# Performance work log

Measured on AMD Instinct MI355X. Metric: run time of the kernel, lower is better.

## Reference

```python
import jax, jax.numpy as jnp
import numpy as np

NEG_BIG = -9e15  # matches torch's -9000000000000000.0 mask value
LEAKY_SLOPE = 0.2  # alpha passed to nn.LeakyReLU


def setup_inputs() -> dict:
    key = jax.random.key(0)
    k1, k2, k3, k4, k5 = jax.random.split(key, 5)
    N, din, de, dout = 500, 100, 200, 100
    return {
        "input_relations": jax.random.normal(k1, (N, din), dtype=jnp.float32),
        "input_entity_embeds": jax.random.normal(k2, (N, N, de), dtype=jnp.float32),
        "relation_adj": jax.random.randint(k3, (N, N), 0, 2, dtype=jnp.int32),
        "a": jax.random.normal(k4, (dout, 2 * din + de), dtype=jnp.float32) * 0.05,
        "a_2": jax.random.normal(k5, (1, dout), dtype=jnp.float32) * 0.05,
    }


def reference(input_relations, input_entity_embeds, relation_adj, a, a_2):
    # Faithful to: a_input[k=(i,j)] = concat(rel_i, rel_j, ent[i,j]); e = a @ a_input
    # We avoid materializing the (N*N, 2*din+de) concat by splitting `a` into the
    # three blocks that hit rel_i, rel_j and ent[i,j] respectively.
    N, din = input_relations.shape
    de = input_entity_embeds.shape[-1]
    a_src = a[:, :din]          # (dout, din) acts on rel_i
    a_dst = a[:, din:2 * din]   # (dout, din) acts on rel_j
    a_ent = a[:, 2 * din:]      # (dout, de)  acts on ent[i,j]

    # e[i, j, o] = a @ concat(rel_i, rel_j, ent_ij)   -> (N, N, dout)
    e = (
        (input_relations @ a_src.T)[:, None, :]
        + (input_relations @ a_dst.T)[None, :, :]
        + jnp.einsum("ijd,od->ijo", input_entity_embeds.reshape(N, N, de), a_ent)
    )

    # scalar score per pair, leaky relu, masked softmax over neighbors j (dim=1)
    e2 = jax.nn.leaky_relu(e @ a_2[0], LEAKY_SLOPE)  # (N, N)
    scores = jnp.where(relation_adj > 0, e2, jnp.float32(NEG_BIG))
    attention = jax.nn.softmax(scores, axis=1)  # (N, N)

    # weighted sum of the score features e (note: original multiplies attention by e,
    # the pre-leakyrelu linear scores, not by a transformed h)
    h_prime = jnp.einsum("ij,ijo->io", attention, e)  # (N, dout)
    return jax.nn.elu(h_prime)  # concat=True branch
```

## Files before the change

### kernel.cpp

```cpp
#include <hip/hip_runtime.h>
#include <stdint.h>
#include <math.h>

#define N     500
#define DIN   100
#define DE    200
#define DOUT  100
#define AROW  (2*DIN + DE)
#define SLOPE 0.2f

#define JCH   4
#define CROWS 125
#define KP    512
#define BK    720
#define DEP   208
#define GZF   104000

typedef __attribute__((ext_vector_type(8)))  short short8;
typedef __attribute__((ext_vector_type(16))) float f32x16;

static __device__ __forceinline__ unsigned short f2bf(float f) {
  union { float f; uint32_t u; } v; v.f = f;
  uint32_t r = (v.u + 0x7FFFu + ((v.u >> 16) & 1u)) >> 16;
  return (unsigned short)r;
}

__global__ __launch_bounds__(256)
void setup_kernel(const float* __restrict__ R, const float* __restrict__ A,
                  const float* __restrict__ a2,
                  float* __restrict__ src, float* __restrict__ ssrc,
                  float* __restrict__ sdst, float* __restrict__ wv,
                  unsigned short* __restrict__ Bcat, unsigned short* __restrict__ Pbuf,
                  float* __restrict__ gsum, float* __restrict__ Zsum) {
  int b = blockIdx.x, t = threadIdx.x;
  if (b < N) {
    int i = b;
    __shared__ float rrow[DIN];
    __shared__ float sred[4];
    if (t < DIN) rrow[t] = R[i * DIN + t];
    if (t < KP - N) Pbuf[i * KP + N + t] = 0;
    __syncthreads();
    int o = -1; bool isSrc = false;
    if (t < DOUT) { o = t; isSrc = true; }
    else if (t >= 128 && t < 128 + DOUT) { o = t - 128; }
    float val = 0.f;
    if (o >= 0) {
      const float* arow = A + o * AROW + (isSrc ? 0 : DIN);
      #pragma unroll 4
      for (int d = 0; d < DIN; ++d) val += rrow[d] * arow[d];
      if (isSrc) src[i * DOUT + o] = val;
      else       Bcat[o * BK + i] = f2bf(val);
    }
    float red = (o >= 0) ? val * a2[o] : 0.f;
    #pragma unroll
    for (int k = 1; k < 64; k <<= 1) red += __shfl_xor(red, k, 64);
    if ((t & 63) == 0) sred[t >> 6] = red;
    __syncthreads();
    if (t == 0)   ssrc[i] = sred[0] + sred[1];
    if (t == 128) sdst[i] = sred[2] + sred[3];
  } else if (b == N) {
    if (t < DE) {
      float s = 0.f;
      for (int o = 0; o < DOUT; ++o) s += A[o * AROW + 2 * DIN + t] * a2[o];
      wv[t] = s;
    }
  } else if (b <= N + DOUT) {
    int o = b - (N + 1);
    if (t < DE) Bcat[o * BK + KP + t] = f2bf(A[o * AROW + 2 * DIN + t]);
    if (t < KP - N) Bcat[o * BK + N + t] = 0;
    if (t >= 32 && t < 32 + (BK - KP - DE)) Bcat[o * BK + KP + DE + (t - 32)] = 0;
  } else if (b <= 702) {
    int off = (b - 601) * 1024 + t * 4;
    if (off < GZF) *(float4*)(gsum + off) = make_float4(0.f, 0.f, 0.f, 0.f);
  } else {
    if (t < 125) *(float4*)(Zsum + t * 4) = make_float4(0.f, 0.f, 0.f, 0.f);
  }
}

__global__ __launch_bounds__(256)
void passA(const float* __restrict__ E, const int* __restrict__ adj,
           const float* __restrict__ ssrcA, const float* __restrict__ sdstA,
           const float* __restrict__ wv,
           unsigned short* __restrict__ Pbuf,
           float* __restrict__ gsum, float* __restrict__ Zsum) {
  __shared__ int list[128];
  __shared__ int cntS;
  __shared__ float gl[4][200];
  __shared__ float zl[4];

  int bid = blockIdx.x;
  int i = bid >> 2, c = bid & 3;
  int jbeg = c * CROWS;
  int t = threadIdx.x, wid = t >> 6, lane = t & 63;

  if (t == 0) cntS = 0;
  __syncthreads();

  bool active = false;
  if (t < CROWS) active = (adj[(size_t)i * N + jbeg + t] > 0);
  unsigned long long mask = __ballot(active);
  int wbase = 0;
  if (lane == 0 && mask) wbase = atomicAdd(&cntS, __popcll(mask));
  wbase = __shfl(wbase, 0);
  if (active) {
    list[wbase + __popcll(mask & ((1ull << lane) - 1ull))] = jbeg + t;
  } else if (t < CROWS) {
    Pbuf[i * KP + jbeg + t] = 0;
  }
  __syncthreads();
  int cnt = cntS;

  float4 w4 = make_float4(0.f, 0.f, 0.f, 0.f);
  if (lane < 50) w4 = *(const float4*)(wv + lane * 4);
  float4 g = make_float4(0.f, 0.f, 0.f, 0.f);
  float Z = 0.f;
  float ssrc_i = ssrcA[i];
  const float* Erow = E + (size_t)i * N * DE;

  for (int base = wid * 4; base + 3 < cnt; base += 16) {
    int j0 = list[base], j1 = list[base + 1], j2 = list[base + 2], j3 = list[base + 3];
    float4 e0 = make_float4(0.f,0.f,0.f,0.f), e1 = e0, e2v = e0, e3 = e0;
    if (lane < 50) {
      e0  = *(const float4*)(Erow + (size_t)j0 * DE + lane * 4);
      e1  = *(const float4*)(Erow + (size_t)j1 * DE + lane * 4);
      e2v = *(const float4*)(Erow + (size_t)j2 * DE + lane * 4);
      e3  = *(const float4*)(Erow + (size_t)j3 * DE + lane * 4);
    }
    float d0 = e0.x*w4.x + e0.y*w4.y + e0.z*w4.z + e0.w*w4.w;
    float d1 = e1.x*w4.x + e1.y*w4.y + e1.z*w4.z + e1.w*w4.w;
    float d2 = e2v.x*w4.x + e2v.y*w4.y + e2v.z*w4.z + e2v.w*w4.w;
    float d3 = e3.x*w4.x + e3.y*w4.y + e3.z*w4.z + e3.w*w4.w;
    #pragma unroll
    for (int k = 1; k < 64; k <<= 1) {
      d0 += __shfl_xor(d0, k); d1 += __shfl_xor(d1, k);
      d2 += __shfl_xor(d2, k); d3 += __shfl_xor(d3, k);
    }
    float s0 = ssrc_i + sdstA[j0] + d0; s0 = s0 > 0.f ? s0 : SLOPE * s0;
    float s1 = ssrc_i + sdstA[j1] + d1; s1 = s1 > 0.f ? s1 : SLOPE * s1;
    float s2 = ssrc_i + sdstA[j2] + d2; s2 = s2 > 0.f ? s2 : SLOPE * s2;
    float s3 = ssrc_i + sdstA[j3] + d3; s3 = s3 > 0.f ? s3 : SLOPE * s3;
    float p0 = __expf(s0), p1 = __expf(s1), p2 = __expf(s2), p3 = __expf(s3);
    Z += (p0 + p1) + (p2 + p3);
    g.x += p0*e0.x + p1*e1.x + p2*e2v.x + p3*e3.x;
    g.y += p0*e0.y + p1*e1.y + p2*e2v.y + p3*e3.y;
    g.z += p0*e0.z + p1*e1.z + p2*e2v.z + p3*e3.z;
    g.w += p0*e0.w + p1*e1.w + p2*e2v.w + p3*e3.w;
    if (lane == 0) {
      Pbuf[i * KP + j0] = f2bf(p0); Pbuf[i * KP + j1] = f2bf(p1);
      Pbuf[i * KP + j2] = f2bf(p2); Pbuf[i * KP + j3] = f2bf(p3);
    }
  }
  for (int idx = (cnt & ~3) + wid; idx < cnt; idx += 4) {
    int j = list[idx];
    float4 ev = make_float4(0.f,0.f,0.f,0.f);
    if (lane < 50) ev = *(const float4*)(Erow + (size_t)j * DE + lane * 4);
    float d = ev.x*w4.x + ev.y*w4.y + ev.z*w4.z + ev.w*w4.w;
    #pragma unroll
    for (int k = 1; k < 64; k <<= 1) d += __shfl_xor(d, k);
    float s = ssrc_i + sdstA[j] + d; s = s > 0.f ? s : SLOPE * s;
    float p = __expf(s);
    Z += p;
    g.x += p*ev.x; g.y += p*ev.y; g.z += p*ev.z; g.w += p*ev.w;
    if (lane == 0) Pbuf[i * KP + j] = f2bf(p);
  }

  if (lane < 50) *(float4*)&gl[wid][lane * 4] = g;
  if (lane == 0) zl[wid] = Z;
  __syncthreads();
  if (t < 200) {
    float s = gl[0][t] + gl[1][t] + gl[2][t] + gl[3][t];
    atomicAdd(gsum + (size_t)i * DEP + t, s);
  }
  if (t == 200) atomicAdd(Zsum + i, zl[0] + zl[1] + zl[2] + zl[3]);
}

__global__ __launch_bounds__(256)
void combine_kernel(const float* __restrict__ src,
                    const unsigned short* __restrict__ Pbuf,
                    const unsigned short* __restrict__ Bcat,
                    const float* __restrict__ gsum,
                    const float* __restrict__ Zsum,
                    float* __restrict__ out) {
  int b = blockIdx.x;
  int t = threadIdx.x;
  int i0 = b * 32;
  int wave = t >> 6, lane = t & 63, c31 = lane & 31, hi = lane >> 5;
  int o = wave * 32 + c31;
  int arow = i0 + c31; if (arow > N - 1) arow = N - 1;

  const unsigned short* Prow = Pbuf + (size_t)arow * KP;
  const float* grow = gsum + (size_t)arow * DEP;

  f32x16 acc = {};
  #pragma unroll
  for (int ks = 0; ks < 45; ++ks) {
    short8 a, bf;
    if (ks < 32) {
      a = *(const short8*)(Prow + ks * 16 + hi * 8);
    } else {
      int d0 = (ks - 32) * 16 + hi * 8;
      float4 ga = *(const float4*)(grow + d0);
      float4 gb = *(const float4*)(grow + d0 + 4);
      a[0] = (short)f2bf(ga.x); a[1] = (short)f2bf(ga.y);
      a[2] = (short)f2bf(ga.z); a[3] = (short)f2bf(ga.w);
      a[4] = (short)f2bf(gb.x); a[5] = (short)f2bf(gb.y);
      a[6] = (short)f2bf(gb.z); a[7] = (short)f2bf(gb.w);
    }
    if (o < DOUT) bf = *(const short8*)(Bcat + (size_t)o * BK + ks * 16 + hi * 8);
    else { short8 zz = {}; bf = zz; }
    acc = __builtin_amdgcn_mfma_f32_32x32x16_bf16(a, bf, acc, 0, 0, 0);
  }

  if (o < DOUT) {
    #pragma unroll
    for (int r = 0; r < 16; ++r) {
      int row = (r & 3) + 8 * (r >> 2) + 4 * hi;
      int i = i0 + row;
      if (i < N) {
        float h = src[i * DOUT + o] + acc[r] / Zsum[i];
        out[i * DOUT + o] = h > 0.f ? h : expm1f(h);
      }
    }
  }
}

extern "C" void kernel_launch(void* const* d_in, const int* in_sizes, int n_in,
                              void* d_out, int out_size, void* d_ws, size_t ws_size,
                              hipStream_t stream) {
  const float* R   = (const float*)d_in[0];
  const float* E   = (const float*)d_in[1];
  const int*   adj = (const int*)d_in[2];
  const float* A   = (const float*)d_in[3];
  const float* a2  = (const float*)d_in[4];
  float* out = (float*)d_out;

  char* wsb = (char*)d_ws;
  float*          src  = (float*)(wsb + 0);
  float*          ssrc = (float*)(wsb + 200000);
  float*          sdst = (float*)(wsb + 202000);
  float*          wv   = (float*)(wsb + 204000);
  unsigned short* Bcat = (unsigned short*)(wsb + 204800);
  unsigned short* Pbuf = (unsigned short*)(wsb + 348800);
  float*          gsum = (float*)(wsb + 860800);
  float*          Zsum = (float*)(wsb + 1276800);

  setup_kernel<<<704, 256, 0, stream>>>(R, A, a2, src, ssrc, sdst, wv, Bcat, Pbuf, gsum, Zsum);
  passA<<<N * JCH, 256, 0, stream>>>(E, adj, ssrc, sdst, wv, Pbuf, gsum, Zsum);
  combine_kernel<<<16, 256, 0, stream>>>(src, Pbuf, Bcat, gsum, Zsum, out);
}
```

Measured before the change: 57.53 us.

## Halve passA blocks per row, unroll 8 neighbors, precompute bias, split combine into waves

passA now splits each row into 2 chunks of 250 instead of 4 of 125. Each wave processes 8 neighbor rows per iteration, which puts more E loads in flight. The per-neighbor bias (ssrc_i + sdst_j) is precomputed into shared memory while the compaction list is built. combine_kernel is relaunched as 64 single-wave blocks instead of 16 four-wave blocks, spreading the MFMA work over more CUs. Risks are higher register pressure from the 8 float4 buffers and fewer blocks for latency hiding in passA.

```diff
diff --git a/kernel.cpp b/kernel.cpp
--- a/kernel.cpp
+++ b/kernel.cpp
@@ -9,8 +9,8 @@
 #define AROW  (2*DIN + DE)
 #define SLOPE 0.2f
 
-#define JCH   4
-#define CROWS 125
+#define JCH   2
+#define CROWS 250
 #define KP    512
 #define BK    720
 #define DEP   208
@@ -77,25 +77,27 @@
   }
 }
 
-__global__ __launch_bounds__(256)
+__global__ __launch_bounds__(256, 4)
 void passA(const float* __restrict__ E, const int* __restrict__ adj,
            const float* __restrict__ ssrcA, const float* __restrict__ sdstA,
            const float* __restrict__ wv,
            unsigned short* __restrict__ Pbuf,
            float* __restrict__ gsum, float* __restrict__ Zsum) {
-  __shared__ int list[128];
+  __shared__ int list[CROWS + 6];
+  __shared__ float bias[CROWS + 6];
   __shared__ int cntS;
   __shared__ float gl[4][200];
   __shared__ float zl[4];
 
   int bid = blockIdx.x;
-  int i = bid >> 2, c = bid & 3;
+  int i = bid >> 1, c = bid & 1;
   int jbeg = c * CROWS;
   int t = threadIdx.x, wid = t >> 6, lane = t & 63;
 
   if (t == 0) cntS = 0;
   __syncthreads();
 
+  float ssrc_i = ssrcA[i];
   bool active = false;
   if (t < CROWS) active = (adj[(size_t)i * N + jbeg + t] > 0);
   unsigned long long mask = __ballot(active);
@@ -103,7 +105,9 @@
   if (lane == 0 && mask) wbase = atomicAdd(&cntS, __popcll(mask));
   wbase = __shfl(wbase, 0);
   if (active) {
-    list[wbase + __popcll(mask & ((1ull << lane) - 1ull))] = jbeg + t;
+    int slot = wbase + __popcll(mask & ((1ull << lane) - 1ull));
+    list[slot] = jbeg + t;
+    bias[slot] = ssrc_i + sdstA[jbeg + t];
   } else if (t < CROWS) {
     Pbuf[i * KP + jbeg + t] = 0;
   }
@@ -114,53 +118,63 @@
   if (lane < 50) w4 = *(const float4*)(wv + lane * 4);
   float4 g = make_float4(0.f, 0.f, 0.f, 0.f);
   float Z = 0.f;
-  float ssrc_i = ssrcA[i];
   const float* Erow = E + (size_t)i * N * DE;
 
-  for (int base = wid * 4; base + 3 < cnt; base += 16) {
-    int j0 = list[base], j1 = list[base + 1], j2 = list[base + 2], j3 = list[base + 3];
-    float4 e0 = make_float4(0.f,0.f,0.f,0.f), e1 = e0, e2v = e0, e3 = e0;
+  for (int base = wid * 8; base + 7 < cnt; base += 32) {
+    int jr[8];
+    float bi[8];
+    #pragma unroll
+    for (int r = 0; r < 8; ++r) { jr[r] = list[base + r]; bi[r] = bias[base + r]; }
+    float4 ev[8];
     if (lane < 50) {
-      e0  = *(const float4*)(Erow + (size_t)j0 * DE + lane * 4);
-      e1  = *(const float4*)(Erow + (size_t)j1 * DE + lane * 4);
-      e2v = *(const float4*)(Erow + (size_t)j2 * DE + lane * 4);
-      e3  = *(const float4*)(Erow + (size_t)j3 * DE + lane * 4);
-    }
-    float d0 = e0.x*w4.x + e0.y*w4.y + e0.z*w4.z + e0.w*w4.w;
-    float d1 = e1.x*w4.x + e1.y*w4.y + e1.z*w4.z + e1.w*w4.w;
-    float d2 = e2v.x*w4.x + e2v.y*w4.y + e2v.z*w4.z + e2v.w*w4.w;
-    float d3 = e3.x*w4.x + e3.y*w4.y + e3.z*w4.z + e3.w*w4.w;
+      #pragma unroll
+      for (int r = 0; r < 8; ++r)
+        ev[r] = *(const float4*)(Erow + (size_t)jr[r] * DE + lane * 4);
+    } else {
+      #pragma unroll
+      for (int r = 0; r < 8; ++r) ev[r] = make_float4(0.f, 0.f, 0.f, 0.f);
+    }
+    float d[8];
+    #pragma unroll
+    for (int r = 0; r < 8; ++r)
+      d[r] = ev[r].x * w4.x + ev[r].y * w4.y + ev[r].z * w4.z + ev[r].w * w4.w;
     #pragma unroll
     for (int k = 1; k < 64; k <<= 1) {
-      d0 += __shfl_xor(d0, k); d1 += __shfl_xor(d1, k);
-      d2 += __shfl_xor(d2, k); d3 += __shfl_xor(d3, k);
-    }
-    float s0 = ssrc_i + sdstA[j0] + d0; s0 = s0 > 0.f ? s0 : SLOPE * s0;
-    float s1 = ssrc_i + sdstA[j1] + d1; s1 = s1 > 0.f ? s1 : SLOPE * s1;
-    float s2 = ssrc_i + sdstA[j2] + d2; s2 = s2 > 0.f ? s2 : SLOPE * s2;
-    float s3 = ssrc_i + sdstA[j3] + d3; s3 = s3 > 0.f ? s3 : SLOPE * s3;
-    float p0 = __expf(s0), p1 = __expf(s1), p2 = __expf(s2), p3 = __expf(s3);
-    Z += (p0 + p1) + (p2 + p3);
-    g.x += p0*e0.x + p1*e1.x + p2*e2v.x + p3*e3.x;
-    g.y += p0*e0.y + p1*e1.y + p2*e2v.y + p3*e3.y;
-    g.z += p0*e0.z + p1*e1.z + p2*e2v.z + p3*e3.z;
-    g.w += p0*e0.w + p1*e1.w + p2*e2v.w + p3*e3.w;
+      #pragma unroll
+      for (int r = 0; r < 8; ++r) d[r] += __shfl_xor(d[r], k);
+    }
+    float p[8];
+    float zacc = 0.f;
+    #pragma unroll
+    for (int r = 0; r < 8; ++r) {
+      float s = bi[r] + d[r];
+      s = s > 0.f ? s : SLOPE * s;
+      p[r] = __expf(s);
+      zacc += p[r];
+    }
+    Z += zacc;
+    #pragma unroll
+    for (int r = 0; r < 8; ++r) {
+      g.x += p[r] * ev[r].x; g.y += p[r] * ev[r].y;
+      g.z += p[r] * ev[r].z; g.w += p[r] * ev[r].w;
+    }
     if (lane == 0) {
-      Pbuf[i * KP + j0] = f2bf(p0); Pbuf[i * KP + j1] = f2bf(p1);
-      Pbuf[i * KP + j2] = f2bf(p2); Pbuf[i * KP + j3] = f2bf(p3);
-    }
-  }
-  for (int idx = (cnt & ~3) + wid; idx < cnt; idx += 4) {
+      #pragma unroll
+      for (int r = 0; r < 8; ++r) Pbuf[i * KP + jr[r]] = f2bf(p[r]);
+    }
+  }
+  for (int idx = (cnt & ~7) + wid; idx < cnt; idx += 4) {
     int j = list[idx];
-    float4 ev = make_float4(0.f,0.f,0.f,0.f);
+    float bi = bias[idx];
+    float4 ev = make_float4(0.f, 0.f, 0.f, 0.f);
     if (lane < 50) ev = *(const float4*)(Erow + (size_t)j * DE + lane * 4);
-    float d = ev.x*w4.x + ev.y*w4.y + ev.z*w4.z + ev.w*w4.w;
+    float d = ev.x * w4.x + ev.y * w4.y + ev.z * w4.z + ev.w * w4.w;
     #pragma unroll
     for (int k = 1; k < 64; k <<= 1) d += __shfl_xor(d, k);
-    float s = ssrc_i + sdstA[j] + d; s = s > 0.f ? s : SLOPE * s;
+    float s = bi + d; s = s > 0.f ? s : SLOPE * s;
     float p = __expf(s);
     Z += p;
-    g.x += p*ev.x; g.y += p*ev.y; g.z += p*ev.z; g.w += p*ev.w;
+    g.x += p * ev.x; g.y += p * ev.y; g.z += p * ev.z; g.w += p * ev.w;
     if (lane == 0) Pbuf[i * KP + j] = f2bf(p);
   }
 
@@ -174,7 +188,7 @@
   if (t == 200) atomicAdd(Zsum + i, zl[0] + zl[1] + zl[2] + zl[3]);
 }
 
-__global__ __launch_bounds__(256)
+__global__ __launch_bounds__(64)
 void combine_kernel(const float* __restrict__ src,
                     const unsigned short* __restrict__ Pbuf,
                     const unsigned short* __restrict__ Bcat,
@@ -182,10 +196,11 @@
                     const float* __restrict__ Zsum,
                     float* __restrict__ out) {
   int b = blockIdx.x;
+  int i0 = (b >> 2) * 32;
+  int ow = b & 3;
   int t = threadIdx.x;
-  int i0 = b * 32;
-  int wave = t >> 6, lane = t & 63, c31 = lane & 31, hi = lane >> 5;
-  int o = wave * 32 + c31;
+  int c31 = t & 31, hi = t >> 5;
+  int o = ow * 32 + c31;
   int arow = i0 + c31; if (arow > N - 1) arow = N - 1;
 
   const unsigned short* Prow = Pbuf + (size_t)arow * KP;
@@ -246,5 +261,5 @@
 
   setup_kernel<<<704, 256, 0, stream>>>(R, A, a2, src, ssrc, sdst, wv, Bcat, Pbuf, gsum, Zsum);
   passA<<<N * JCH, 256, 0, stream>>>(E, adj, ssrc, sdst, wv, Pbuf, gsum, Zsum);
-  combine_kernel<<<16, 256, 0, stream>>>(src, Pbuf, Bcat, gsum, Zsum, out);
-}
+  combine_kernel<<<64, 64, 0, stream>>>(src, Pbuf, Bcat, gsum, Zsum, out);
+}
```

Result: faster. 54.86 us (-4.6%).
